# Kernel tuning notes

Measured on AMD Instinct MI355X. Metric: run time of the kernel, lower is better.

## Reference

```python
import jax, jax.numpy as jnp
import numpy as np

N_HEADS = 16

def setup_inputs() -> dict:
    key = jax.random.key(0)
    ks = jax.random.split(key, 6)
    B, S, D = 2, 2048, 1024
    return {
        "hidden_states": jax.random.normal(ks[0], (B, S, D), dtype=jnp.float32),
        "Wq": jax.random.normal(ks[1], (D, D), dtype=jnp.float32) * (1.0 / np.sqrt(D)),
        "Wk": jax.random.normal(ks[2], (D, D), dtype=jnp.float32) * (1.0 / np.sqrt(D)),
        "Wv": jax.random.normal(ks[3], (D, D), dtype=jnp.float32) * (1.0 / np.sqrt(D)),
        "Wo": jax.random.normal(ks[4], (D, D), dtype=jnp.float32) * (1.0 / np.sqrt(D)),
        "bo": jnp.zeros((D,), dtype=jnp.float32),
    }

def reference(hidden_states, Wq, Wk, Wv, Wo, bo):
    B, S, D = hidden_states.shape
    H = N_HEADS
    hd = D // H  # head_dim; d_kv == d_model per module's final view
    # nn.Linear(bias=False): x @ W.T, then the module's direct view to (B, H, S, hd)
    q = (hidden_states @ Wq.T).reshape(B, H, S, hd)
    k = (hidden_states @ Wk.T).reshape(B, H, S, hd)  # self-attention path (encoder_states=None)
    v = (hidden_states @ Wv.T).reshape(B, H, S, hd)
    # naive full score matrix [B, H, S, S]
    wei = jnp.einsum('bhqd,bhkd->bhqk', q, k)
    causal = jnp.tril(jnp.ones((S, S), dtype=bool))
    wei = jnp.where(causal, wei, -jnp.inf)
    # NOTE: module divides logits by head_dim (not sqrt) -- preserved faithfully
    attn = jax.nn.softmax(wei / hd, axis=-1)
    ctx = jnp.einsum('bhqk,bhkd->bhqd', attn, v)  # [B, H, S, hd]
    out = ctx.transpose(0, 2, 1, 3).reshape(B, S, D)
    return out @ Wo.T + bo
```

## Files before the change

### kernel.cpp

```cpp
#include <hip/hip_runtime.h>

#define S_LEN   2048
#define D_MODEL 1024
#define N_HEADS 16
#define HEAD_DIM 64

typedef unsigned short u16;
typedef float  floatx4 __attribute__((ext_vector_type(4)));
typedef short  bf16x8  __attribute__((ext_vector_type(8)));
typedef short  bf16x4  __attribute__((ext_vector_type(4)));

__device__ __forceinline__ u16 f2bf(float f) {
    unsigned int u = __float_as_uint(f);
    u += 0x7FFF + ((u >> 16) & 1);
    return (u16)(u >> 16);
}
__device__ __forceinline__ unsigned pack2bf(float a, float b) {
    return (unsigned)f2bf(a) | ((unsigned)f2bf(b) << 16);
}

__device__ __forceinline__ void gload_lds16(const void* g, void* l) {
    __builtin_amdgcn_global_load_lds(
        reinterpret_cast<const __attribute__((address_space(1))) unsigned int*>(
            reinterpret_cast<uintptr_t>(g)),
        reinterpret_cast<__attribute__((address_space(3))) unsigned int*>(
            reinterpret_cast<uintptr_t>(l)),
        16, 0, 0);
}

__global__ __launch_bounds__(256) void cast_all(const float* __restrict__ hs,
                                                const float* __restrict__ w0,
                                                const float* __restrict__ w1,
                                                const float* __restrict__ w2,
                                                const float* __restrict__ w3,
                                                u16* __restrict__ dst) {
    const size_t NHS = (size_t)2 * S_LEN * D_MODEL;
    const size_t e0 = (size_t)blockIdx.x * 2048;
    const float* src;
    size_t base;
    if (e0 < NHS)                 { src = hs; base = 0; }
    else {
        const int wi = (int)((e0 - NHS) >> 20);
        src = wi == 0 ? w0 : wi == 1 ? w1 : wi == 2 ? w2 : w3;
        base = NHS + ((size_t)wi << 20);
    }
    const size_t i = e0 + (size_t)threadIdx.x * 8;
    const float4 a = *(const float4*)(src + (i - base));
    const float4 b = *(const float4*)(src + (i - base) + 4);
    uint4 o;
    o.x = pack2bf(a.x, a.y); o.y = pack2bf(a.z, a.w);
    o.z = pack2bf(b.x, b.y); o.w = pack2bf(b.z, b.w);
    *(uint4*)(dst + i) = o;
}

__global__ __launch_bounds__(256) void vtrans(const u16* __restrict__ Vf,
                                              u16* __restrict__ Vt) {
    __shared__ unsigned T[64 * 133];
    const int bh = blockIdx.y;
    const int sBase = blockIdx.x * 128;
    const u16* src = Vf + (size_t)bh * (S_LEN * HEAD_DIM) + (size_t)sBase * HEAD_DIM;
    u16* dst = Vt + (size_t)bh * (S_LEN * HEAD_DIM) + sBase;
    const int tid = threadIdx.x;

#pragma unroll
    for (int it = 0; it < 4; ++it) {
        const int idx = it * 256 + tid;
        const int row = idx >> 3, ch = idx & 7;
        const float4 v4 = *(const float4*)(src + row * 64 + ch * 8);
        const u16* vs = (const u16*)&v4;
#pragma unroll
        for (int j = 0; j < 8; ++j) T[(ch * 8 + j) * 133 + row] = vs[j];
    }
    __syncthreads();
#pragma unroll
    for (int it = 0; it < 4; ++it) {
        const int idx = it * 256 + tid;
        const int d = idx >> 4, sc = idx & 15;
        union { u16 u[8]; float4 f; } tmp;
#pragma unroll
        for (int j = 0; j < 8; ++j) tmp.u[j] = (u16)T[d * 133 + sc * 8 + j];
        *(float4*)(dst + (size_t)d * S_LEN + sc * 8) = tmp.f;
    }
}

__global__ __launch_bounds__(256) void gemm_qkv(const u16* __restrict__ A,
                                                const u16* __restrict__ Wq,
                                                const u16* __restrict__ Wk,
                                                const u16* __restrict__ Wv,
                                                u16* __restrict__ Qo,
                                                u16* __restrict__ Ko,
                                                u16* __restrict__ Vfo) {
    __shared__ u16 As[8 * 512];
    __shared__ u16 Ws[8 * 512];

    const int blk = blockIdx.x;
    const int y   = (blk & 7) | (((blk >> 3) & 3) << 3);
    const int x   = blk >> 5;
    const int which = x >> 3;
    const int nBase = (x & 7) * 128;
    const int mBase = y * 128;
    const u16* W = which == 0 ? Wq : which == 1 ? Wk : Wv;

    const int tid = threadIdx.x, lane = tid & 63, wv = tid >> 6;
    const int l15 = lane & 15, quad = lane >> 4;
    const int wm = wv & 1, wn = wv >> 1;
    const int srow = lane >> 2;
    const int gch  = (lane & 3) ^ ((lane >> 3) & 3);
    const int swz  = (l15 >> 1) & 3;

    floatx4 acc[4][4];
#pragma unroll
    for (int i = 0; i < 4; ++i)
#pragma unroll
        for (int j = 0; j < 4; ++j) acc[i][j] = (floatx4)(0.0f);

    for (int k0 = 0; k0 < D_MODEL; k0 += 32) {
        __syncthreads();
#pragma unroll
        for (int t = 0; t < 2; ++t) {
            const int ci = wv * 2 + t;
            gload_lds16(A + (size_t)(mBase + ci * 16 + srow) * D_MODEL + k0 + gch * 8,
                        &As[ci * 512]);
            gload_lds16(W + (size_t)(nBase + ci * 16 + srow) * D_MODEL + k0 + gch * 8,
                        &Ws[ci * 512]);
        }
        __syncthreads();

        bf16x8 af[4], bfr[4];
#pragma unroll
        for (int mt = 0; mt < 4; ++mt)
            af[mt] = *(const bf16x8*)&As[(wm * 64 + mt * 16 + l15) * 32 + (quad ^ swz) * 8];
#pragma unroll
        for (int nt = 0; nt < 4; ++nt)
            bfr[nt] = *(const bf16x8*)&Ws[(wn * 64 + nt * 16 + l15) * 32 + (quad ^ swz) * 8];
#pragma unroll
        for (int mt = 0; mt < 4; ++mt)
#pragma unroll
            for (int nt = 0; nt < 4; ++nt)
                acc[mt][nt] = __builtin_amdgcn_mfma_f32_16x16x32_bf16(af[mt], bfr[nt], acc[mt][nt], 0, 0, 0);
    }

    u16* O = which == 0 ? Qo : (which == 1 ? Ko : Vfo);
    const float scale = which == 0 ? (1.44269504088896f / 64.0f) : 1.0f;
#pragma unroll
    for (int mt = 0; mt < 4; ++mt)
#pragma unroll
        for (int nt = 0; nt < 4; ++nt) {
            const int col = nBase + wn * 64 + nt * 16 + l15;
#pragma unroll
            for (int r = 0; r < 4; ++r) {
                const int row = mBase + wm * 64 + mt * 16 + quad * 4 + r;
                O[(size_t)row * D_MODEL + col] = f2bf(acc[mt][nt][r] * scale);
            }
        }
}

__global__ __launch_bounds__(256) void gemm_out(const u16* __restrict__ A,
                                                const u16* __restrict__ W,
                                                const float* __restrict__ bias,
                                                float* __restrict__ C) {
    __shared__ u16 As[4 * 512];
    __shared__ u16 Ws[8 * 512];

    const int nBase = blockIdx.x * 128;
    const int mBase = blockIdx.y * 64;
    const int tid = threadIdx.x, lane = tid & 63, wv = tid >> 6;
    const int l15 = lane & 15, quad = lane >> 4;
    const int wm = wv & 1, wn = wv >> 1;
    const int srow = lane >> 2;
    const int gch  = (lane & 3) ^ ((lane >> 3) & 3);
    const int swz  = (l15 >> 1) & 3;

    floatx4 acc[2][4];
#pragma unroll
    for (int i = 0; i < 2; ++i)
#pragma unroll
        for (int j = 0; j < 4; ++j) acc[i][j] = (floatx4)(0.0f);

    for (int k0 = 0; k0 < D_MODEL; k0 += 32) {
        __syncthreads();
        gload_lds16(A + (size_t)(mBase + wv * 16 + srow) * D_MODEL + k0 + gch * 8,
                    &As[wv * 512]);
#pragma unroll
        for (int t = 0; t < 2; ++t) {
            const int ci = wv * 2 + t;
            gload_lds16(W + (size_t)(nBase + ci * 16 + srow) * D_MODEL + k0 + gch * 8,
                        &Ws[ci * 512]);
        }
        __syncthreads();

        bf16x8 af[2], bfr[4];
#pragma unroll
        for (int mt = 0; mt < 2; ++mt)
            af[mt] = *(const bf16x8*)&As[(wm * 32 + mt * 16 + l15) * 32 + (quad ^ swz) * 8];
#pragma unroll
        for (int nt = 0; nt < 4; ++nt)
            bfr[nt] = *(const bf16x8*)&Ws[(wn * 64 + nt * 16 + l15) * 32 + (quad ^ swz) * 8];
#pragma unroll
        for (int mt = 0; mt < 2; ++mt)
#pragma unroll
            for (int nt = 0; nt < 4; ++nt)
                acc[mt][nt] = __builtin_amdgcn_mfma_f32_16x16x32_bf16(af[mt], bfr[nt], acc[mt][nt], 0, 0, 0);
    }

#pragma unroll
    for (int mt = 0; mt < 2; ++mt)
#pragma unroll
        for (int nt = 0; nt < 4; ++nt) {
            const int col = nBase + wn * 64 + nt * 16 + l15;
            const float bv = bias[col];
#pragma unroll
            for (int r = 0; r < 4; ++r) {
                const int row = mBase + wm * 32 + mt * 16 + quad * 4 + r;
                C[(size_t)row * D_MODEL + col] = acc[mt][nt][r] + bv;
            }
        }
}

__global__ __launch_bounds__(256, 3) void attn6(const u16* __restrict__ Q,
                                                const u16* __restrict__ K,
                                                const u16* __restrict__ Vt,
                                                u16* __restrict__ Ctx) {
    __shared__ u16 Ks[4096];
    __shared__ u16 Vs[4096];
    __shared__ float RedA[64 * 68];
    __shared__ float RedB[64 * 68];
    __shared__ float lpbuf[4 * 64];

    const int flat = blockIdx.x;
    const int g    = flat & 31;
    const int qt   = 31 - (flat >> 5);
    const int h = g & 15, b = g >> 4;

    const int tid = threadIdx.x, lane = tid & 63, wv = tid >> 6;
    const int l15 = lane & 15, quad = lane >> 4;

    const size_t headOff = ((size_t)b * N_HEADS + h) * S_LEN * HEAD_DIM;
    const u16* Qh = Q + headOff;
    const u16* Kh = K + headOff;
    const u16* Vh = Vt + headOff;
    u16* Cb = Ctx + (size_t)b * S_LEN * D_MODEL + (size_t)h * HEAD_DIM;

    const int srow = lane >> 3;
    const int gch  = (lane & 7) ^ srow;
    const int swz  = l15 & 7;

    const int qBase = qt * 64;

    bf16x8 qb[4][2];
#pragma unroll
    for (int qg = 0; qg < 4; ++qg)
#pragma unroll
        for (int ks = 0; ks < 2; ++ks)
            qb[qg][ks] = *(const bf16x8*)(Qh + (size_t)(qBase + qg * 16 + l15) * 64
                                          + ks * 32 + quad * 8);

    floatx4 o[4][4];
#pragma unroll
    for (int qg = 0; qg < 4; ++qg)
#pragma unroll
        for (int dg = 0; dg < 4; ++dg) o[qg][dg] = (floatx4)(0.0f);
    float lp[4] = {0.0f, 0.0f, 0.0f, 0.0f};

    for (int kt = 0; kt <= qt; ++kt) {
        const int kBase = kt * 64;
        __syncthreads();
#pragma unroll
        for (int t = 0; t < 2; ++t) {
            const int ci = wv * 2 + t;
            gload_lds16(Kh + (size_t)(kBase + ci * 8 + srow) * 64 + gch * 8, &Ks[ci * 512]);
            gload_lds16(Vh + (size_t)(ci * 8 + srow) * S_LEN + kBase + gch * 8, &Vs[ci * 512]);
        }
        __syncthreads();

        bf16x8 ka[2];
#pragma unroll
        for (int ks = 0; ks < 2; ++ks)
            ka[ks] = *(const bf16x8*)&Ks[(wv * 16 + l15) * 64 + ((ks * 4 + quad) ^ swz) * 8];

        bf16x4 vb[4];
#pragma unroll
        for (int dg = 0; dg < 4; ++dg)
            vb[dg] = *(const bf16x4*)&Vs[(dg * 16 + l15) * 64
                                         + (((wv * 2 + (quad >> 1)) ^ swz) * 8) + (quad & 1) * 4];

        floatx4 s[4];
#pragma unroll
        for (int qg = 0; qg < 4; ++qg) {
            s[qg] = (floatx4)(0.0f);
#pragma unroll
            for (int ks = 0; ks < 2; ++ks)
                s[qg] = __builtin_amdgcn_mfma_f32_16x16x32_bf16(ka[ks], qb[qg][ks], s[qg], 0, 0, 0);
        }

        const bool diag = (kt == qt);
#pragma unroll
        for (int qg = 0; qg < 4; ++qg) {
            if (diag && qg < wv) continue;
            float p[4];
#pragma unroll
            for (int r = 0; r < 4; ++r) {
                float pv = __builtin_amdgcn_exp2f(s[qg][r]);
                if (diag && qg == wv && (quad * 4 + r > l15)) pv = 0.0f;
                p[r] = pv;
                lp[qg] += pv;
            }
            union { uint2 u; bf16x4 v; } pk;
            pk.u.x = __builtin_amdgcn_perm(__float_as_uint(p[1]), __float_as_uint(p[0]), 0x07060302);
            pk.u.y = __builtin_amdgcn_perm(__float_as_uint(p[3]), __float_as_uint(p[2]), 0x07060302);
#pragma unroll
            for (int dg = 0; dg < 4; ++dg)
                o[qg][dg] = __builtin_amdgcn_mfma_f32_16x16x16bf16_1k(pk.v, vb[dg], o[qg][dg], 0, 0, 0);
        }
    }

#pragma unroll
    for (int qg = 0; qg < 4; ++qg) {
        lp[qg] += __shfl_xor(lp[qg], 16);
        lp[qg] += __shfl_xor(lp[qg], 32);
    }
    lpbuf[wv * 64 + quad * 16 + l15] = lp[quad];

    if (wv == 1 || wv == 3) {
        float* R = (wv == 1) ? RedA : RedB;
#pragma unroll
        for (int qg = 0; qg < 4; ++qg)
#pragma unroll
            for (int dg = 0; dg < 4; ++dg)
                *(floatx4*)&R[(dg * 16 + l15) * 68 + qg * 16 + quad * 4] = o[qg][dg];
    }
    __syncthreads();
    if (wv == 0 || wv == 2) {
        const float* R = (wv == 0) ? RedA : RedB;
#pragma unroll
        for (int qg = 0; qg < 4; ++qg)
#pragma unroll
            for (int dg = 0; dg < 4; ++dg)
                o[qg][dg] += *(const floatx4*)&R[(dg * 16 + l15) * 68 + qg * 16 + quad * 4];
    }
    __syncthreads();
    if (wv == 2) {
#pragma unroll
        for (int qg = 0; qg < 4; ++qg)
#pragma unroll
            for (int dg = 0; dg < 4; ++dg)
                *(floatx4*)&RedA[(dg * 16 + l15) * 68 + qg * 16 + quad * 4] = o[qg][dg];
    }
    __syncthreads();
    if (wv == 0) {
#pragma unroll
        for (int qg = 0; qg < 4; ++qg) {
#pragma unroll
            for (int dg = 0; dg < 4; ++dg)
                o[qg][dg] += *(const floatx4*)&RedA[(dg * 16 + l15) * 68 + qg * 16 + quad * 4];
            floatx4 lt = *(const floatx4*)&lpbuf[0 * 64 + qg * 16 + quad * 4];
            lt += *(const floatx4*)&lpbuf[1 * 64 + qg * 16 + quad * 4];
            lt += *(const floatx4*)&lpbuf[2 * 64 + qg * 16 + quad * 4];
            lt += *(const floatx4*)&lpbuf[3 * 64 + qg * 16 + quad * 4];
#pragma unroll
            for (int r = 0; r < 4; ++r) {
                const float inv = 1.0f / lt[r];
                const int row = qBase + qg * 16 + quad * 4 + r;
#pragma unroll
                for (int dg = 0; dg < 4; ++dg)
                    Cb[(size_t)row * D_MODEL + dg * 16 + l15] = f2bf(o[qg][dg][r] * inv);
            }
        }
    }
}

extern "C" void kernel_launch(void* const* d_in, const int* in_sizes, int n_in,
                              void* d_out, int out_size, void* d_ws, size_t ws_size,
                              hipStream_t stream) {
    const float* hs = (const float*)d_in[0];
    const float* Wq = (const float*)d_in[1];
    const float* Wk = (const float*)d_in[2];
    const float* Wv = (const float*)d_in[3];
    const float* Wo = (const float*)d_in[4];
    const float* bo = (const float*)d_in[5];
    float* out = (float*)d_out;

    const size_t NHS = (size_t)2 * S_LEN * D_MODEL;
    const size_t NW  = (size_t)D_MODEL * D_MODEL;

    u16* hsb = (u16*)d_ws;
    u16* Wb  = hsb + NHS;
    u16* Qb  = Wb + 4 * NW;
    u16* Kb  = Qb + NHS;
    u16* Vfb = Kb + NHS;
    u16* Vtb = Vfb + NHS;
    u16* Cxb = Vtb + NHS;

    cast_all<<<4096, 256, 0, stream>>>(hs, Wq, Wk, Wv, Wo, hsb);

    gemm_qkv<<<768, 256, 0, stream>>>(hsb, Wb, Wb + NW, Wb + 2 * NW,
                                      Qb, Kb, Vfb);

    vtrans<<<dim3(16, 32), 256, 0, stream>>>(Vfb, Vtb);

    attn6<<<1024, 256, 0, stream>>>(Qb, Kb, Vtb, Cxb);

    gemm_out<<<dim3(8, 64), 256, 0, stream>>>(Cxb, Wb + 3 * NW, bo, out);
}
```

Baseline: 172.3 us.

## Double-buffer K/V tiles in attention kernel to overlap loads with compute

Switches the attention kernel's K and V LDS tiles to two buffers. The next tile is prefetched with global_load_lds while the current one is consumed, leaving one barrier per iteration instead of two. The reduction buffers are aliased onto the same shared memory to cap LDS usage near its previous size. There is a risk of races because the async LDS loads are not explicitly waited on before the trailing barrier. The reduction buffers also overlap the K/V buffers after the loop.

```diff
diff --git a/kernel.cpp b/kernel.cpp
--- a/kernel.cpp
+++ b/kernel.cpp
@@ -221,11 +221,12 @@
                                                 const u16* __restrict__ K,
                                                 const u16* __restrict__ Vt,
                                                 u16* __restrict__ Ctx) {
-    __shared__ u16 Ks[4096];
-    __shared__ u16 Vs[4096];
-    __shared__ float RedA[64 * 68];
-    __shared__ float RedB[64 * 68];
-    __shared__ float lpbuf[4 * 64];
+    __shared__ __align__(16) char smem[35840];
+    u16*   Ks    = (u16*)smem;
+    u16*   Vs    = (u16*)(smem + 16384);
+    float* RedA  = (float*)smem;
+    float* RedB  = (float*)(smem + 17408);
+    float* lpbuf = (float*)(smem + 34816);
 
     const int flat = blockIdx.x;
     const int g    = flat & 31;
@@ -262,26 +263,39 @@
         for (int dg = 0; dg < 4; ++dg) o[qg][dg] = (floatx4)(0.0f);
     float lp[4] = {0.0f, 0.0f, 0.0f, 0.0f};
 
+#pragma unroll
+    for (int t = 0; t < 2; ++t) {
+        const int ci = wv * 2 + t;
+        gload_lds16(Kh + (size_t)(ci * 8 + srow) * 64 + gch * 8, &Ks[ci * 512]);
+        gload_lds16(Vh + (size_t)(ci * 8 + srow) * S_LEN + gch * 8, &Vs[ci * 512]);
+    }
+    __syncthreads();
+
     for (int kt = 0; kt <= qt; ++kt) {
-        const int kBase = kt * 64;
-        __syncthreads();
-#pragma unroll
-        for (int t = 0; t < 2; ++t) {
-            const int ci = wv * 2 + t;
-            gload_lds16(Kh + (size_t)(kBase + ci * 8 + srow) * 64 + gch * 8, &Ks[ci * 512]);
-            gload_lds16(Vh + (size_t)(ci * 8 + srow) * S_LEN + kBase + gch * 8, &Vs[ci * 512]);
-        }
-        __syncthreads();
+        const int cur = (kt & 1) * 4096;
+        const int nxt = 4096 - cur;
+
+        if (kt < qt) {
+            const int kB2 = (kt + 1) * 64;
+#pragma unroll
+            for (int t = 0; t < 2; ++t) {
+                const int ci = wv * 2 + t;
+                gload_lds16(Kh + (size_t)(kB2 + ci * 8 + srow) * 64 + gch * 8,
+                            &Ks[nxt + ci * 512]);
+                gload_lds16(Vh + (size_t)(ci * 8 + srow) * S_LEN + kB2 + gch * 8,
+                            &Vs[nxt + ci * 512]);
+            }
+        }
 
         bf16x8 ka[2];
 #pragma unroll
         for (int ks = 0; ks < 2; ++ks)
-            ka[ks] = *(const bf16x8*)&Ks[(wv * 16 + l15) * 64 + ((ks * 4 + quad) ^ swz) * 8];
+            ka[ks] = *(const bf16x8*)&Ks[cur + (wv * 16 + l15) * 64 + ((ks * 4 + quad) ^ swz) * 8];
 
         bf16x4 vb[4];
 #pragma unroll
         for (int dg = 0; dg < 4; ++dg)
-            vb[dg] = *(const bf16x4*)&Vs[(dg * 16 + l15) * 64
+            vb[dg] = *(const bf16x4*)&Vs[cur + (dg * 16 + l15) * 64
                                          + (((wv * 2 + (quad >> 1)) ^ swz) * 8) + (quad & 1) * 4];
 
         floatx4 s[4];
@@ -312,6 +326,8 @@
             for (int dg = 0; dg < 4; ++dg)
                 o[qg][dg] = __builtin_amdgcn_mfma_f32_16x16x16bf16_1k(pk.v, vb[dg], o[qg][dg], 0, 0, 0);
         }
+
+        __syncthreads();
     }
 
 #pragma unroll
```

Measured after the change: 168.5 us. -2.2%, faster.
